# Kernel optimization log

Measured on AMD Instinct MI355X. Metric: run time of the kernel, lower is better.

Reference implementation:

```python
import jax, jax.numpy as jnp
import numpy as np

H = 256      # hidden_dim
NH = 4       # num_heads
DK = H // NH # per-head dim
NL = 2       # num self-attn layers
TL = 6       # transformer_num_layers (output repeat)
PTS_DIM = 3


def _layer_norm(x, g, b, eps=1e-5):
    m = jnp.mean(x, axis=-1, keepdims=True)
    v = jnp.mean((x - m) ** 2, axis=-1, keepdims=True)
    return (x - m) / jnp.sqrt(v + eps) * g + b


def _mha(x, Wq, bq, Wk, bk, Wv, bv, Wo, bo, g, bb, bias):
    # x: [B,N,H]; bias: [B,NH,N,N]; way='add' (att_spm_type='add')
    B, N, _ = x.shape
    q = (x @ Wq + bq).reshape(B, N, NH, DK).transpose(0, 2, 1, 3)  # [B,h,N,d]
    k = (x @ Wk + bk).reshape(B, N, NH, DK).transpose(0, 2, 1, 3)
    v = (x @ Wv + bv).reshape(B, N, NH, DK).transpose(0, 2, 1, 3)
    att = jnp.einsum('bhnd,bhmd->bhnm', q, k) / np.sqrt(DK).astype(np.float32)
    att = jax.nn.softmax(att + bias, axis=-1)
    out = jnp.einsum('bhnm,bhmd->bhnd', att, v).transpose(0, 2, 1, 3).reshape(B, N, H)
    out = out @ Wo + bo
    return _layer_norm(x + out, g, bb)


def setup_inputs() -> dict:
    key = jax.random.key(0)
    ks = jax.random.split(key, 16)
    B, N = 1, 512
    s = 0.02  # weight init scale
    inp = {
        'history_states': jax.random.normal(ks[0], (TL, B, N, H), jnp.float32),
        'all_lanes_preds': jax.random.normal(ks[1], (TL, B, N, 33), jnp.float32),
        'fc_W': jax.random.normal(ks[2], (H, H), jnp.float32) * s,
        'fc_b': jnp.zeros((H,), jnp.float32),
        'Wq': jax.random.normal(ks[3], (NL, H, H), jnp.float32) * s,
        'bq': jnp.zeros((NL, H), jnp.float32),
        'Wk': jax.random.normal(ks[4], (NL, H, H), jnp.float32) * s,
        'bk': jnp.zeros((NL, H), jnp.float32),
        'Wv': jax.random.normal(ks[5], (NL, H, H), jnp.float32) * s,
        'bv': jnp.zeros((NL, H), jnp.float32),
        'Wo': jax.random.normal(ks[6], (NL, H, H), jnp.float32) * s,
        'bo': jnp.zeros((NL, H), jnp.float32),
        'ln_g': jnp.ones((NL, H), jnp.float32),
        'ln_b': jnp.zeros((NL, H), jnp.float32),
        'mlp1_W': jax.random.normal(ks[7], (H, H), jnp.float32) * s,
        'mlp1_b': jnp.zeros((H,), jnp.float32),
        'mlp2_W': jax.random.normal(ks[8], (H, H), jnp.float32) * s,
        'mlp2_b': jnp.zeros((H,), jnp.float32),
        'cls_W1': jax.random.normal(ks[9], (2 * H, H), jnp.float32) * s,
        'cls_b1': jnp.zeros((H,), jnp.float32),
        'cls_W2': jax.random.normal(ks[10], (H, 1), jnp.float32) * s,
        'cls_b2': jnp.zeros((1,), jnp.float32),
    }
    return inp


def reference(history_states, all_lanes_preds, fc_W, fc_b, Wq, bq, Wk, bk, Wv, bv,
              Wo, bo, ln_g, ln_b, mlp1_W, mlp1_b, mlp2_W, mlp2_b,
              cls_W1, cls_b1, cls_W2, cls_b2):
    query_feats = history_states[-1]                 # [B,N,H]
    coords = all_lanes_preds[-1]                      # [B,N,33]
    B, N, C = coords.shape
    coords = coords.reshape(B, N, C // PTS_DIM, PTS_DIM)
    query_end_point = coords[:, :, -1, :]             # [B,N,3]
    key_start_point = coords[:, :, 0, :]              # [B,N,3]

    # pairwise distance bias: dist[b,i,j] = ||key_start[j] - query_end[i]||
    diff = key_start_point[:, None, :, :] - query_end_point[:, :, None, :]
    dist = jnp.sqrt(jnp.sum(diff ** 2, axis=-1))[:, None, :, :]  # [B,1,N,N]
    dw = 1.0 / (dist + 0.01)
    dw = dw / jnp.sum(dw, axis=2, keepdims=True)      # normalize over dim 2
    zeros = jnp.zeros_like(dw)
    dist_weights = jax.lax.stop_gradient(
        jnp.concatenate([dw, -dist, zeros, zeros], axis=1))  # [B,4,N,N]

    # features_concat: Linear + ReLU
    x = jax.nn.relu(query_feats @ fc_W + fc_b)

    for i in range(NL):
        x = _mha(x, Wq[i], bq[i], Wk[i], bk[i], Wv[i], bv[i],
                 Wo[i], bo[i], ln_g[i], ln_b[i], dist_weights)

    # lclc relationship head: per-side MLP, pairwise concat, classifier
    o1 = jax.nn.relu(x @ mlp1_W + mlp1_b)             # [B,N,H]
    o2 = jax.nn.relu(x @ mlp2_W + mlp2_b)
    pair = jnp.concatenate([
        jnp.broadcast_to(o1[:, :, None, :], (B, N, N, H)),
        jnp.broadcast_to(o2[:, None, :, :], (B, N, N, H))], axis=-1)  # [B,N,N,2H]
    z = jax.nn.relu(pair @ cls_W1 + cls_b1)
    lclc = (z @ cls_W2 + cls_b2)[..., 0]              # [B,N,N]
    all_lclc_preds = jnp.broadcast_to(lclc[None], (TL, B, N, N))
    return all_lclc_preds
```

## Files before the change

### kernel.cpp

```cpp
#include <hip/hip_runtime.h>
#include <math.h>


#define NTOK 512
#define HDIM 256
#define DKH  64
#define NHEAD 4
#define TLEN 6
#define WSZ  65536
#define PSTR 520
#define XPS  264

typedef __attribute__((ext_vector_type(8))) short bf16x8;
typedef __attribute__((ext_vector_type(4))) float f32x4;

__device__ __forceinline__ ushort f2bf(float f)
{
    unsigned u = __builtin_bit_cast(unsigned, f);
    u += 0x7FFFu + ((u >> 16) & 1u);
    return (ushort)(u >> 16);
}

struct PKArg {
    const float* w[13];
    const float* pl;
    ushort* wpk;
    float *dist, *dwraw, *inv_cs;
};

__global__ __launch_bounds__(256) void pack_kernel(PKArg p)
{
    __shared__ __align__(16) ushort smu[64 * 72];
    const int bid = blockIdx.x;
    const int t   = threadIdx.x;

    if (bid < 208) {
        const int mat  = bid >> 4;
        const int tile = bid & 15;
        const int k0   = (tile >> 2) * 64;
        const int c0   = (tile & 3) * 64;
        const float* W = p.w[mat];
#pragma unroll
        for (int j = 0; j < 4; ++j) {
            const int i  = t + j * 256;
            const int r  = i >> 4, c4 = i & 15;
            const float4 v4 = *(const float4*)&W[(k0 + r) * HDIM + c0 + c4 * 4];
            smu[(c4 * 4 + 0) * 72 + r] = f2bf(v4.x);
            smu[(c4 * 4 + 1) * 72 + r] = f2bf(v4.y);
            smu[(c4 * 4 + 2) * 72 + r] = f2bf(v4.z);
            smu[(c4 * 4 + 3) * 72 + r] = f2bf(v4.w);
        }
        __syncthreads();
#pragma unroll
        for (int j = 0; j < 2; ++j) {
            const int i  = t + j * 256;
            const int cr = i >> 3, kk = i & 7;
            const uint4 v = *(const uint4*)&smu[cr * 72 + kk * 8];
            *(uint4*)&p.wpk[mat * WSZ + (c0 + cr) * HDIM + k0 + kk * 8] = v;
        }
    } else {
        float* smf = (float*)smu;
        float* qe  = smf;
        float* red = smf + 1536;
        const int item = bid - 208;
        for (int i = t; i < 512; i += 256) {
            qe[i * 3 + 0] = p.pl[i * 33 + 30];
            qe[i * 3 + 1] = p.pl[i * 33 + 31];
            qe[i * 3 + 2] = p.pl[i * 33 + 32];
        }
        __syncthreads();
        const int m   = item * 64 + (t & 63);
        const int nch = t >> 6;
        const float kx = p.pl[m * 33 + 0], ky = p.pl[m * 33 + 1], kz = p.pl[m * 33 + 2];
        float cs = 0.f;
        for (int n = nch * 128; n < nch * 128 + 128; ++n) {
            const float dx = kx - qe[n * 3 + 0];
            const float dy = ky - qe[n * 3 + 1];
            const float dz = kz - qe[n * 3 + 2];
            const float dd = sqrtf(dx * dx + dy * dy + dz * dz);
            const float w  = 1.0f / (dd + 0.01f);
            p.dist[n * NTOK + m]  = dd;
            p.dwraw[n * NTOK + m] = w;
            cs += w;
        }
        red[nch * 64 + (t & 63)] = cs;
        __syncthreads();
        if (t < 64)
            p.inv_cs[item * 64 + t] =
                1.0f / (red[t] + red[64 + t] + red[128 + t] + red[192 + t]);
    }
}

__device__ __forceinline__ void qkv_one2(
    const ushort* __restrict__ xpan, const ushort* __restrict__ Wt,
    const float* __restrict__ bb, int prob,
    int slab, int c0, int lr, int lg, int lk,
    ushort* __restrict__ q16, ushort* __restrict__ k16,
    ushort* __restrict__ vT16)
{
    const ushort* Ap = xpan + lr * XPS + lk;
    f32x4 acc[2];
    acc[0] = (f32x4){0.f, 0.f, 0.f, 0.f};
    acc[1] = (f32x4){0.f, 0.f, 0.f, 0.f};
#pragma unroll
    for (int ks = 0; ks < 8; ++ks) {
        const bf16x8 a = *(const bf16x8*)&Ap[ks * 32];
#pragma unroll
        for (int j = 0; j < 2; ++j) {
            const bf16x8 b = *(const bf16x8*)&Wt[(c0 + j * 16 + lr) * HDIM + ks * 32 + lk];
            acc[j] = __builtin_amdgcn_mfma_f32_16x16x32_bf16(a, b, acc[j], 0, 0, 0);
        }
    }
#pragma unroll
    for (int j = 0; j < 2; ++j) {
        const int col = c0 + j * 16 + lr;
        const float bv2 = bb[col];
        if (prob < 2) {
            ushort* dst = (prob == 0) ? q16 : k16;
#pragma unroll
            for (int rg = 0; rg < 4; ++rg)
                dst[(slab + lg * 4 + rg) * HDIM + col] = f2bf(acc[j][rg] + bv2);
        } else {
            ushort4 s = {f2bf(acc[j][0] + bv2), f2bf(acc[j][1] + bv2),
                         f2bf(acc[j][2] + bv2), f2bf(acc[j][3] + bv2)};
            *(ushort4*)&vT16[col * NTOK + slab + lg * 4] = s;
        }
    }
}

__global__ __launch_bounds__(256) void fcqkv(
    const float* __restrict__ qf, const ushort* __restrict__ fcWt,
    const float* __restrict__ fcb,
    const ushort* __restrict__ WqT, const float* __restrict__ bq,
    const ushort* __restrict__ WkT, const float* __restrict__ bk,
    const ushort* __restrict__ WvT, const float* __restrict__ bv,
    float* __restrict__ xa, ushort* __restrict__ q16,
    ushort* __restrict__ k16, ushort* __restrict__ vT16)
{
    __shared__ __align__(16) ushort xpan[16 * XPS];
    const int bid  = blockIdx.x;
    const int p6   = bid >> 5;
    const int slab = (bid & 31) * 16;
    const int t = threadIdx.x;
    const int wv = t >> 6, lane = t & 63;
    const int lr = lane & 15, lg = lane >> 4, lk = lg * 8;
    const int c0 = wv * 64;

    {
        f32x4 acc[4];
#pragma unroll
        for (int j = 0; j < 4; ++j) acc[j] = (f32x4){0.f, 0.f, 0.f, 0.f};
        const float* Aq = qf + (slab + lr) * HDIM + lk;
#pragma unroll
        for (int ks = 0; ks < 8; ++ks) {
            const float4 a0 = *(const float4*)&Aq[ks * 32];
            const float4 a1 = *(const float4*)&Aq[ks * 32 + 4];
            bf16x8 a;
            a[0] = (short)f2bf(a0.x); a[1] = (short)f2bf(a0.y);
            a[2] = (short)f2bf(a0.z); a[3] = (short)f2bf(a0.w);
            a[4] = (short)f2bf(a1.x); a[5] = (short)f2bf(a1.y);
            a[6] = (short)f2bf(a1.z); a[7] = (short)f2bf(a1.w);
#pragma unroll
            for (int j = 0; j < 4; ++j) {
                const bf16x8 b = *(const bf16x8*)&fcWt[(c0 + j * 16 + lr) * HDIM + ks * 32 + lk];
                acc[j] = __builtin_amdgcn_mfma_f32_16x16x32_bf16(a, b, acc[j], 0, 0, 0);
            }
        }
#pragma unroll
        for (int j = 0; j < 4; ++j) {
            const int col = c0 + j * 16 + lr;
            const float bbv = fcb[col];
#pragma unroll
            for (int rg = 0; rg < 4; ++rg) {
                const float o = fmaxf(acc[j][rg] + bbv, 0.f);
                if (p6 == 0) xa[(slab + lg * 4 + rg) * HDIM + col] = o;
                xpan[(lg * 4 + rg) * XPS + col] = f2bf(o);
            }
        }
    }
    __syncthreads();
    const int prob = p6 >> 1, ch = p6 & 1;
    const ushort* Wt = (prob == 0) ? WqT : (prob == 1) ? WkT : WvT;
    const float*  bb = (prob == 0) ? bq  : (prob == 1) ? bk  : bv;
    qkv_one2(xpan, Wt, bb, prob, slab, ch * 128 + wv * 32, lr, lg, lk,
             q16, k16, vT16);
}

__global__ __launch_bounds__(512) void attn_fused(
    const ushort* __restrict__ q16, const ushort* __restrict__ k16,
    const ushort* __restrict__ vT16, const float* __restrict__ dist,
    const float* __restrict__ dwraw, const float* __restrict__ inv_cs,
    ushort* __restrict__ ao16)
{
    __shared__ __align__(16) ushort P_lds[16 * PSTR];
    __shared__ __align__(16) float exch[8][16][64];
    __shared__ float rmax[8][16];
    __shared__ float psums[8][16];

    const int bid = blockIdx.x;
    const int h  = bid >> 5;
    const int n0 = (bid & 31) * 16;
    const int t  = threadIdx.x;
    const int wv = t >> 6, lane = t & 63;
    const int lr = lane & 15, lg = lane >> 4, lk = lg * 8;
    const int mW = wv * 64;

    const ushort* Qrow = q16 + (n0 + lr) * HDIM + h * DKH + lk;
    const bf16x8 a0 = *(const bf16x8*)&Qrow[0];
    const bf16x8 a1 = *(const bf16x8*)&Qrow[32];

    f32x4 accs[4];
#pragma unroll
    for (int cg = 0; cg < 4; ++cg) accs[cg] = (f32x4){0.f, 0.f, 0.f, 0.f};
#pragma unroll
    for (int cg = 0; cg < 4; ++cg) {
        const ushort* Brow = k16 + (mW + cg * 16 + lr) * HDIM + h * DKH + lk;
        accs[cg] = __builtin_amdgcn_mfma_f32_16x16x32_bf16(
            a0, *(const bf16x8*)&Brow[0], accs[cg], 0, 0, 0);
        accs[cg] = __builtin_amdgcn_mfma_f32_16x16x32_bf16(
            a1, *(const bf16x8*)&Brow[32], accs[cg], 0, 0, 0);
    }

    float s[4][4];
#pragma unroll
    for (int cg = 0; cg < 4; ++cg) {
        const int m = mW + cg * 16 + lr;
        const float ic = (h == 0) ? inv_cs[m] : 0.f;
#pragma unroll
        for (int rg = 0; rg < 4; ++rg) {
            const int n = n0 + lg * 4 + rg;
            float b = 0.f;
            if (h == 0)      b = dwraw[n * NTOK + m] * ic;
            else if (h == 1) b = -dist[n * NTOK + m];
            s[cg][rg] = accs[cg][rg] * 0.125f + b;
        }
    }

    float mx[4];
#pragma unroll
    for (int rg = 0; rg < 4; ++rg) {
        float m = fmaxf(fmaxf(s[0][rg], s[1][rg]), fmaxf(s[2][rg], s[3][rg]));
#pragma unroll
        for (int o = 1; o < 16; o <<= 1) m = fmaxf(m, __shfl_xor(m, o));
        mx[rg] = m;
    }
    if (lr == 0)
#pragma unroll
        for (int rg = 0; rg < 4; ++rg) rmax[wv][lg * 4 + rg] = mx[rg];
    __syncthreads();
    float mxf[4];
#pragma unroll
    for (int rg = 0; rg < 4; ++rg) {
        const int row = lg * 4 + rg;
        float m = rmax[0][row];
#pragma unroll
        for (int w = 1; w < 8; ++w) m = fmaxf(m, rmax[w][row]);
        mxf[rg] = m;
    }

    float ps[4] = {0.f, 0.f, 0.f, 0.f};
#pragma unroll
    for (int cg = 0; cg < 4; ++cg)
#pragma unroll
        for (int rg = 0; rg < 4; ++rg) {
            const float e = __expf(s[cg][rg] - mxf[rg]);
            ps[rg] += e;
            P_lds[(lg * 4 + rg) * PSTR + mW + cg * 16 + lr] = f2bf(e);
        }
#pragma unroll
    for (int rg = 0; rg < 4; ++rg) {
#pragma unroll
        for (int o = 1; o < 16; o <<= 1) ps[rg] += __shfl_xor(ps[rg], o);
    }
    if (lr == 0)
#pragma unroll
        for (int rg = 0; rg < 4; ++rg) psums[wv][lg * 4 + rg] = ps[rg];
    __syncthreads();

    f32x4 acco[4];
#pragma unroll
    for (int db = 0; db < 4; ++db) acco[db] = (f32x4){0.f, 0.f, 0.f, 0.f};
#pragma unroll
    for (int c = 0; c < 2; ++c) {
        const bf16x8 pa = *(const bf16x8*)&P_lds[lr * PSTR + mW + c * 32 + lk];
#pragma unroll
        for (int db = 0; db < 4; ++db) {
            const bf16x8 b = *(const bf16x8*)
                &vT16[(h * DKH + db * 16 + lr) * NTOK + mW + c * 32 + lk];
            acco[db] = __builtin_amdgcn_mfma_f32_16x16x32_bf16(pa, b, acco[db], 0, 0, 0);
        }
    }
#pragma unroll
    for (int db = 0; db < 4; ++db)
#pragma unroll
        for (int rg = 0; rg < 4; ++rg)
            exch[wv][lg * 4 + rg][db * 16 + lr] = acco[db][rg];
    __syncthreads();

    {
        const int r = t >> 5, dp = (t & 31) * 2;
        float sx = 0.f, sy = 0.f, den = 0.f;
#pragma unroll
        for (int w = 0; w < 8; ++w) {
            const float2 e = *(const float2*)&exch[w][r][dp];
            sx += e.x; sy += e.y;
            den += psums[w][r];
        }
        const float inv = 1.0f / den;
        ushort2 o = {f2bf(sx * inv), f2bf(sy * inv)};
        *(ushort2*)&ao16[(n0 + r) * HDIM + h * DKH + dp] = o;
    }
}

__device__ __forceinline__ void oprojln_phase(
    const ushort* __restrict__ ao16, const ushort* __restrict__ WoT,
    const float* __restrict__ bo, const float* __restrict__ gamma,
    const float* __restrict__ beta, const float* __restrict__ x,
    int slab, int c0, int wv, int lr, int lg, int lk,
    float red[4][16], f32x4 acc[4])
{
    const ushort* Arow = ao16 + (slab + lr) * HDIM + lk;
#pragma unroll
    for (int j = 0; j < 4; ++j) acc[j] = (f32x4){0.f, 0.f, 0.f, 0.f};
#pragma unroll
    for (int ks = 0; ks < 8; ++ks) {
        const bf16x8 a = *(const bf16x8*)&Arow[ks * 32];
#pragma unroll
        for (int j = 0; j < 4; ++j) {
            const bf16x8 b = *(const bf16x8*)&WoT[(c0 + j * 16 + lr) * HDIM + ks * 32 + lk];
            acc[j] = __builtin_amdgcn_mfma_f32_16x16x32_bf16(a, b, acc[j], 0, 0, 0);
        }
    }
#pragma unroll
    for (int j = 0; j < 4; ++j) {
        const int col = c0 + j * 16 + lr;
        const float bc = bo[col];
#pragma unroll
        for (int rg = 0; rg < 4; ++rg)
            acc[j][rg] += bc + x[(slab + lg * 4 + rg) * HDIM + col];
    }

    float sm[4];
#pragma unroll
    for (int rg = 0; rg < 4; ++rg) {
        float s = 0.f;
#pragma unroll
        for (int j = 0; j < 4; ++j) s += acc[j][rg];
#pragma unroll
        for (int o = 1; o < 16; o <<= 1) s += __shfl_xor(s, o);
        sm[rg] = s;
    }
    if (lr == 0)
#pragma unroll
        for (int rg = 0; rg < 4; ++rg) red[wv][lg * 4 + rg] = sm[rg];
    __syncthreads();
    float mean[4];
#pragma unroll
    for (int rg = 0; rg < 4; ++rg) {
        const int row = lg * 4 + rg;
        mean[rg] = (red[0][row] + red[1][row] + red[2][row] + red[3][row]) * (1.f / 256.f);
    }
    __syncthreads();

#pragma unroll
    for (int rg = 0; rg < 4; ++rg) {
        float s2 = 0.f;
#pragma unroll
        for (int j = 0; j < 4; ++j) {
            const float c = acc[j][rg] - mean[rg];
            s2 += c * c;
        }
#pragma unroll
        for (int o = 1; o < 16; o <<= 1) s2 += __shfl_xor(s2, o);
        sm[rg] = s2;
    }
    if (lr == 0)
#pragma unroll
        for (int rg = 0; rg < 4; ++rg) red[wv][lg * 4 + rg] = sm[rg];
    __syncthreads();
    float rstd[4];
#pragma unroll
    for (int rg = 0; rg < 4; ++rg) {
        const int row = lg * 4 + rg;
        const float var = (red[0][row] + red[1][row] + red[2][row] + red[3][row]) * (1.f / 256.f);
        rstd[rg] = rsqrtf(var + 1e-5f);
    }
#pragma unroll
    for (int j = 0; j < 4; ++j) {
        const int col = c0 + j * 16 + lr;
        const float gg = gamma[col], bv = beta[col];
#pragma unroll
        for (int rg = 0; rg < 4; ++rg)
            acc[j][rg] = (acc[j][rg] - mean[rg]) * rstd[rg] * gg + bv;
    }
}

__global__ __launch_bounds__(256) void oprojqkv(
    const ushort* __restrict__ ao16, const ushort* __restrict__ WoT,
    const float* __restrict__ bo, const float* __restrict__ gamma,
    const float* __restrict__ beta,
    const ushort* __restrict__ WqT, const float* __restrict__ bq,
    const ushort* __restrict__ WkT, const float* __restrict__ bk,
    const ushort* __restrict__ WvT, const float* __restrict__ bv,
    const float* __restrict__ xa, float* __restrict__ xb,
    ushort* __restrict__ q16, ushort* __restrict__ k16,
    ushort* __restrict__ vT16)
{
    __shared__ __align__(16) ushort xpan[16 * XPS];
    __shared__ float red[4][16];
    const int bid  = blockIdx.x;
    const int p6   = bid >> 5;
    const int slab = (bid & 31) * 16;
    const int t = threadIdx.x;
    const int wv = t >> 6, lane = t & 63;
    const int lr = lane & 15, lg = lane >> 4, lk = lg * 8;
    const int c0 = wv * 64;

    f32x4 acc[4];
    oprojln_phase(ao16, WoT, bo, gamma, beta, xa, slab, c0, wv, lr, lg, lk, red, acc);
#pragma unroll
    for (int j = 0; j < 4; ++j) {
        const int col = c0 + j * 16 + lr;
#pragma unroll
        for (int rg = 0; rg < 4; ++rg) {
            if (p6 == 0) xb[(slab + lg * 4 + rg) * HDIM + col] = acc[j][rg];
            xpan[(lg * 4 + rg) * XPS + col] = f2bf(acc[j][rg]);
        }
    }
    __syncthreads();
    const int prob = p6 >> 1, ch = p6 & 1;
    const ushort* Wt = (prob == 0) ? WqT : (prob == 1) ? WkT : WvT;
    const float*  bb = (prob == 0) ? bq  : (prob == 1) ? bk  : bv;
    qkv_one2(xpan, Wt, bb, prob, slab, ch * 128 + wv * 32, lr, lg, lk,
             q16, k16, vT16);
}

__global__ __launch_bounds__(256) void oprojmlpU(
    const ushort* __restrict__ ao16, const ushort* __restrict__ WoT,
    const float* __restrict__ bo, const float* __restrict__ gamma,
    const float* __restrict__ beta,
    const ushort* __restrict__ m1WT, const float* __restrict__ m1b,
    const ushort* __restrict__ m2WT, const float* __restrict__ m2b,
    const ushort* __restrict__ cW1aT, const float* __restrict__ cb1,
    const ushort* __restrict__ cW1bT,
    const float* __restrict__ xb, float* __restrict__ U1, float* __restrict__ U2)
{
    __shared__ __align__(16) ushort xpan[16 * XPS];
    __shared__ __align__(16) ushort opan[16 * XPS];
    __shared__ float red[4][16];
    const int bid  = blockIdx.x;
    const int p4   = bid >> 5;
    const int p    = p4 >> 1, ch = p4 & 1;
    const int slab = (bid & 31) * 16;
    const int t = threadIdx.x;
    const int wv = t >> 6, lane = t & 63;
    const int lr = lane & 15, lg = lane >> 4, lk = lg * 8;
    const int c0 = wv * 64;

    f32x4 acc[4];
    oprojln_phase(ao16, WoT, bo, gamma, beta, xb, slab, c0, wv, lr, lg, lk, red, acc);
#pragma unroll
    for (int j = 0; j < 4; ++j) {
        const int col = c0 + j * 16 + lr;
#pragma unroll
        for (int rg = 0; rg < 4; ++rg)
            xpan[(lg * 4 + rg) * XPS + col] = f2bf(acc[j][rg]);
    }
    __syncthreads();

    {
        const ushort* Wt = p ? m2WT : m1WT;
        const float*  bb = p ? m2b  : m1b;
        const ushort* Ap = xpan + lr * XPS + lk;
        f32x4 a2[4];
#pragma unroll
        for (int j = 0; j < 4; ++j) a2[j] = (f32x4){0.f, 0.f, 0.f, 0.f};
#pragma unroll
        for (int ks = 0; ks < 8; ++ks) {
            const bf16x8 a = *(const bf16x8*)&Ap[ks * 32];
#pragma unroll
            for (int j = 0; j < 4; ++j) {
                const bf16x8 b = *(const bf16x8*)&Wt[(c0 + j * 16 + lr) * HDIM + ks * 32 + lk];
                a2[j] = __builtin_amdgcn_mfma_f32_16x16x32_bf16(a, b, a2[j], 0, 0, 0);
            }
        }
#pragma unroll
        for (int j = 0; j < 4; ++j) {
            const int col = c0 + j * 16 + lr;
            const float bbv = bb[col];
#pragma unroll
            for (int rg = 0; rg < 4; ++rg)
                opan[(lg * 4 + rg) * XPS + col] = f2bf(fmaxf(a2[j][rg] + bbv, 0.f));
        }
    }
    __syncthreads();

    {
        const ushort* Wt = p ? cW1bT : cW1aT;
        float* U         = p ? U2 : U1;
        const int cb     = ch * 128 + wv * 32;
        const ushort* Ao = opan + lr * XPS + lk;
        f32x4 a2[2];
        a2[0] = (f32x4){0.f, 0.f, 0.f, 0.f};
        a2[1] = (f32x4){0.f, 0.f, 0.f, 0.f};
#pragma unroll
        for (int ks = 0; ks < 8; ++ks) {
            const bf16x8 a = *(const bf16x8*)&Ao[ks * 32];
#pragma unroll
            for (int j = 0; j < 2; ++j) {
                const bf16x8 b = *(const bf16x8*)&Wt[(cb + j * 16 + lr) * HDIM + ks * 32 + lk];
                a2[j] = __builtin_amdgcn_mfma_f32_16x16x32_bf16(a, b, a2[j], 0, 0, 0);
            }
        }
#pragma unroll
        for (int j = 0; j < 2; ++j) {
            const int col = cb + j * 16 + lr;
            const float bbv = (p == 0) ? cb1[col] : 0.f;
#pragma unroll
            for (int rg = 0; rg < 4; ++rg)
                U[(slab + lg * 4 + rg) * HDIM + col] = a2[j][rg] + bbv;
        }
    }
}

__global__ __launch_bounds__(256) void pair_cls(const float* __restrict__ U1,
                                                const float* __restrict__ U2,
                                                const float* __restrict__ W2,
                                                const float* __restrict__ b2,
                                                float* __restrict__ out)
{
    __shared__ __align__(16) float u1s[32][260];
    __shared__ __align__(16) float u2s[32][260];
    __shared__ __align__(16) float w2s[256];
    const int t  = threadIdx.x;
    const int n0 = blockIdx.y * 32, m0 = blockIdx.x * 32;

    for (int i = t; i < 32 * 64; i += 256) {
        const int r = i >> 6, c4 = i & 63;
        *(float4*)&u1s[r][c4 * 4] = *(const float4*)&U1[(n0 + r) * HDIM + c4 * 4];
        *(float4*)&u2s[r][c4 * 4] = *(const float4*)&U2[(m0 + r) * HDIM + c4 * 4];
    }
    if (t < 64) *(float4*)&w2s[t * 4] = *(const float4*)&W2[t * 4];
    __syncthreads();

    const int tx = t & 15, ty = t >> 4;
    float acc[2][2] = {};
    for (int h4 = 0; h4 < 64; ++h4) {
        const float4 a0 = *(const float4*)&u1s[ty * 2][h4 * 4];
        const float4 a1 = *(const float4*)&u1s[ty * 2 + 1][h4 * 4];
        const float4 b0 = *(const float4*)&u2s[tx * 2][h4 * 4];
        const float4 b1 = *(const float4*)&u2s[tx * 2 + 1][h4 * 4];
        const float4 w  = *(const float4*)&w2s[h4 * 4];
#define RT(A, B) fmaxf((A) + (B), 0.f)
        acc[0][0] += RT(a0.x,b0.x)*w.x + RT(a0.y,b0.y)*w.y + RT(a0.z,b0.z)*w.z + RT(a0.w,b0.w)*w.w;
        acc[0][1] += RT(a0.x,b1.x)*w.x + RT(a0.y,b1.y)*w.y + RT(a0.z,b1.z)*w.z + RT(a0.w,b1.w)*w.w;
        acc[1][0] += RT(a1.x,b0.x)*w.x + RT(a1.y,b0.y)*w.y + RT(a1.z,b0.z)*w.z + RT(a1.w,b0.w)*w.w;
        acc[1][1] += RT(a1.x,b1.x)*w.x + RT(a1.y,b1.y)*w.y + RT(a1.z,b1.z)*w.z + RT(a1.w,b1.w)*w.w;
#undef RT
    }
    const float bbv = b2[0];
#pragma unroll
    for (int ii = 0; ii < 2; ++ii)
#pragma unroll
        for (int jj = 0; jj < 2; ++jj) {
            const float val = acc[ii][jj] + bbv;
            const int n = n0 + ty * 2 + ii;
            const int m = m0 + tx * 2 + jj;
#pragma unroll
            for (int tl = 0; tl < TLEN; ++tl)
                out[tl * NTOK * NTOK + n * NTOK + m] = val;
        }
}

extern "C" void kernel_launch(void* const* d_in, const int* in_sizes, int n_in,
                              void* d_out, int out_size, void* d_ws, size_t ws_size,
                              hipStream_t stream)
{
    const float* hs   = (const float*)d_in[0];
    const float* qf   = hs + 5 * NTOK * HDIM;
    const float* alp  = (const float*)d_in[1];
    const float* pl   = alp + 5 * NTOK * 33;
    const float* fc_W = (const float*)d_in[2];
    const float* fc_b = (const float*)d_in[3];
    const float* Wq   = (const float*)d_in[4];
    const float* bq   = (const float*)d_in[5];
    const float* Wk   = (const float*)d_in[6];
    const float* bk   = (const float*)d_in[7];
    const float* Wv   = (const float*)d_in[8];
    const float* bv   = (const float*)d_in[9];
    const float* Wo   = (const float*)d_in[10];
    const float* bo   = (const float*)d_in[11];
    const float* lng  = (const float*)d_in[12];
    const float* lnb  = (const float*)d_in[13];
    const float* m1W  = (const float*)d_in[14];
    const float* m1b  = (const float*)d_in[15];
    const float* m2W  = (const float*)d_in[16];
    const float* m2b  = (const float*)d_in[17];
    const float* cW1  = (const float*)d_in[18];
    const float* cb1  = (const float*)d_in[19];
    const float* cW2  = (const float*)d_in[20];
    const float* cb2  = (const float*)d_in[21];
    float* out = (float*)d_out;

    const int NN  = NTOK * NTOK;
    const int NH_ = NTOK * HDIM;
    float* ws     = (float*)d_ws;
    float* dist   = ws;
    float* dwraw  = ws + NN;
    float* inv_cs = ws + 2 * NN;
    float* xa     = ws + 2 * NN + 512;
    float* xb     = xa + NH_;
    float* U1     = xb + NH_;
    float* U2     = U1 + NH_;
    ushort* u16   = (ushort*)(U2 + NH_);
    ushort* wpk   = u16;
    ushort* q16   = wpk + 13 * WSZ;
    ushort* k16   = q16 + NH_;
    ushort* vT16  = k16 + NH_;
    ushort* ao16  = vT16 + NH_;

    PKArg pk;
    pk.w[0]  = fc_W;
    pk.w[1]  = Wq;  pk.w[2]  = Wq + WSZ;
    pk.w[3]  = Wk;  pk.w[4]  = Wk + WSZ;
    pk.w[5]  = Wv;  pk.w[6]  = Wv + WSZ;
    pk.w[7]  = Wo;  pk.w[8]  = Wo + WSZ;
    pk.w[9]  = m1W; pk.w[10] = m2W;
    pk.w[11] = cW1; pk.w[12] = cW1 + WSZ;
    pk.pl = pl;
    pk.wpk = wpk;
    pk.dist = dist; pk.dwraw = dwraw; pk.inv_cs = inv_cs;
    pack_kernel<<<216, 256, 0, stream>>>(pk);

    fcqkv<<<192, 256, 0, stream>>>(
        qf, wpk + 0 * WSZ, fc_b,
        wpk + 1 * WSZ, bq, wpk + 3 * WSZ, bk, wpk + 5 * WSZ, bv,
        xa, q16, k16, vT16);

    attn_fused<<<128, 512, 0, stream>>>(q16, k16, vT16, dist, dwraw, inv_cs, ao16);

    oprojqkv<<<192, 256, 0, stream>>>(
        ao16, wpk + 7 * WSZ, bo, lng, lnb,
        wpk + 2 * WSZ, bq + HDIM, wpk + 4 * WSZ, bk + HDIM,
        wpk + 6 * WSZ, bv + HDIM,
        xa, xb, q16, k16, vT16);

    attn_fused<<<128, 512, 0, stream>>>(q16, k16, vT16, dist, dwraw, inv_cs, ao16);

    oprojmlpU<<<128, 256, 0, stream>>>(
        ao16, wpk + 8 * WSZ, bo + HDIM, lng + HDIM, lnb + HDIM,
        wpk + 9 * WSZ, m1b, wpk + 10 * WSZ, m2b,
        wpk + 11 * WSZ, cb1, wpk + 12 * WSZ,
        xb, U1, U2);

    pair_cls<<<dim3(16, 16), 256, 0, stream>>>(U1, U2, cW2, cb2, out);
}
```

Before: 97.69 us.

## Store pair-head U1/U2 as bf16 and repartition attention PV across waves

The U1/U2 intermediates produced by oprojmlpU are now stored as bf16 and unpacked to fp32 in pair_cls. This halves their global traffic and the LDS footprint of the pair tile, at some cost in precision. In attn_fused, each wave now owns one 16-column slice of the head dim over half of the keys instead of all 64 columns over 64 keys. That shrinks the cross-wave exchange buffer from 8 partials to 2 and uses wider final stores. The change trades more unpack ALU work in the pair loop for less memory and LDS traffic.

```diff
diff --git a/kernel.cpp b/kernel.cpp
--- a/kernel.cpp
+++ b/kernel.cpp
@@ -19,6 +19,14 @@
     unsigned u = __builtin_bit_cast(unsigned, f);
     u += 0x7FFFu + ((u >> 16) & 1u);
     return (ushort)(u >> 16);
+}
+__device__ __forceinline__ float bf_lo(unsigned u)
+{
+    return __builtin_bit_cast(float, u << 16);
+}
+__device__ __forceinline__ float bf_hi(unsigned u)
+{
+    return __builtin_bit_cast(float, u & 0xFFFF0000u);
 }
 
 struct PKArg {
@@ -193,7 +201,7 @@
     ushort* __restrict__ ao16)
 {
     __shared__ __align__(16) ushort P_lds[16 * PSTR];
-    __shared__ __align__(16) float exch[8][16][64];
+    __shared__ __align__(16) float exch[2][16][64];
     __shared__ float rmax[8][16];
     __shared__ float psums[8][16];
 
@@ -277,38 +285,34 @@
         for (int rg = 0; rg < 4; ++rg) psums[wv][lg * 4 + rg] = ps[rg];
     __syncthreads();
 
-    f32x4 acco[4];
-#pragma unroll
-    for (int db = 0; db < 4; ++db) acco[db] = (f32x4){0.f, 0.f, 0.f, 0.f};
-#pragma unroll
-    for (int c = 0; c < 2; ++c) {
-        const bf16x8 pa = *(const bf16x8*)&P_lds[lr * PSTR + mW + c * 32 + lk];
-#pragma unroll
-        for (int db = 0; db < 4; ++db) {
-            const bf16x8 b = *(const bf16x8*)
-                &vT16[(h * DKH + db * 16 + lr) * NTOK + mW + c * 32 + lk];
-            acco[db] = __builtin_amdgcn_mfma_f32_16x16x32_bf16(pa, b, acco[db], 0, 0, 0);
-        }
-    }
-#pragma unroll
-    for (int db = 0; db < 4; ++db)
+    {
+        const int db = wv & 3, kh = wv >> 2;
+        f32x4 acco = (f32x4){0.f, 0.f, 0.f, 0.f};
+        const ushort* Vrow = vT16 + (h * DKH + db * 16 + lr) * NTOK + kh * 256 + lk;
+        const ushort* Prow = P_lds + lr * PSTR + kh * 256 + lk;
+#pragma unroll
+        for (int c = 0; c < 8; ++c) {
+            const bf16x8 pa = *(const bf16x8*)&Prow[c * 32];
+            const bf16x8 b  = *(const bf16x8*)&Vrow[c * 32];
+            acco = __builtin_amdgcn_mfma_f32_16x16x32_bf16(pa, b, acco, 0, 0, 0);
+        }
 #pragma unroll
         for (int rg = 0; rg < 4; ++rg)
-            exch[wv][lg * 4 + rg][db * 16 + lr] = acco[db][rg];
-    __syncthreads();
-
-    {
-        const int r = t >> 5, dp = (t & 31) * 2;
-        float sx = 0.f, sy = 0.f, den = 0.f;
-#pragma unroll
-        for (int w = 0; w < 8; ++w) {
-            const float2 e = *(const float2*)&exch[w][r][dp];
-            sx += e.x; sy += e.y;
-            den += psums[w][r];
-        }
+            exch[kh][lg * 4 + rg][db * 16 + lr] = acco[rg];
+    }
+    __syncthreads();
+
+    if (t < 256) {
+        const int r = t >> 4, d4 = t & 15;
+        f32x4 sum = *(const f32x4*)&exch[0][r][d4 * 4];
+        sum += *(const f32x4*)&exch[1][r][d4 * 4];
+        float den = 0.f;
+#pragma unroll
+        for (int w = 0; w < 8; ++w) den += psums[w][r];
         const float inv = 1.0f / den;
-        ushort2 o = {f2bf(sx * inv), f2bf(sy * inv)};
-        *(ushort2*)&ao16[(n0 + r) * HDIM + h * DKH + dp] = o;
+        ushort4 o = {f2bf(sum.x * inv), f2bf(sum.y * inv),
+                     f2bf(sum.z * inv), f2bf(sum.w * inv)};
+        *(ushort4*)&ao16[(n0 + r) * HDIM + h * DKH + d4 * 4] = o;
     }
 }
 
@@ -443,7 +447,8 @@
     const ushort* __restrict__ m2WT, const float* __restrict__ m2b,
     const ushort* __restrict__ cW1aT, const float* __restrict__ cb1,
     const ushort* __restrict__ cW1bT,
-    const float* __restrict__ xb, float* __restrict__ U1, float* __restrict__ U2)
+    const float* __restrict__ xb, ushort* __restrict__ U1b,
+    ushort* __restrict__ U2b)
 {
     __shared__ __align__(16) ushort xpan[16 * XPS];
     __shared__ __align__(16) ushort opan[16 * XPS];
@@ -497,7 +502,7 @@
 
     {
         const ushort* Wt = p ? cW1bT : cW1aT;
-        float* U         = p ? U2 : U1;
+        ushort* U        = p ? U2b : U1b;
         const int cb     = ch * 128 + wv * 32;
         const ushort* Ao = opan + lr * XPS + lk;
         f32x4 a2[2];
@@ -518,46 +523,68 @@
             const float bbv = (p == 0) ? cb1[col] : 0.f;
 #pragma unroll
             for (int rg = 0; rg < 4; ++rg)
-                U[(slab + lg * 4 + rg) * HDIM + col] = a2[j][rg] + bbv;
-        }
-    }
-}
-
-__global__ __launch_bounds__(256) void pair_cls(const float* __restrict__ U1,
-                                                const float* __restrict__ U2,
+                U[(slab + lg * 4 + rg) * HDIM + col] = f2bf(a2[j][rg] + bbv);
+        }
+    }
+}
+
+__global__ __launch_bounds__(256) void pair_cls(const ushort* __restrict__ U1b,
+                                                const ushort* __restrict__ U2b,
                                                 const float* __restrict__ W2,
                                                 const float* __restrict__ b2,
                                                 float* __restrict__ out)
 {
-    __shared__ __align__(16) float u1s[32][260];
-    __shared__ __align__(16) float u2s[32][260];
+    __shared__ __align__(16) ushort u1s[32][264];
+    __shared__ __align__(16) ushort u2s[32][264];
     __shared__ __align__(16) float w2s[256];
     const int t  = threadIdx.x;
     const int n0 = blockIdx.y * 32, m0 = blockIdx.x * 32;
 
-    for (int i = t; i < 32 * 64; i += 256) {
-        const int r = i >> 6, c4 = i & 63;
-        *(float4*)&u1s[r][c4 * 4] = *(const float4*)&U1[(n0 + r) * HDIM + c4 * 4];
-        *(float4*)&u2s[r][c4 * 4] = *(const float4*)&U2[(m0 + r) * HDIM + c4 * 4];
+#pragma unroll
+    for (int u = 0; u < 4; ++u) {
+        const int i = t + u * 256;
+        const int r = i >> 5, c8 = i & 31;
+        *(uint4*)&u1s[r][c8 * 8] = *(const uint4*)&U1b[(n0 + r) * HDIM + c8 * 8];
+        *(uint4*)&u2s[r][c8 * 8] = *(const uint4*)&U2b[(m0 + r) * HDIM + c8 * 8];
     }
     if (t < 64) *(float4*)&w2s[t * 4] = *(const float4*)&W2[t * 4];
     __syncthreads();
 
     const int tx = t & 15, ty = t >> 4;
+    const ushort* r0 = &u1s[ty * 2][0];
+    const ushort* r1 = &u1s[ty * 2 + 1][0];
+    const ushort* c0 = &u2s[tx * 2][0];
+    const ushort* c1 = &u2s[tx * 2 + 1][0];
     float acc[2][2] = {};
-    for (int h4 = 0; h4 < 64; ++h4) {
-        const float4 a0 = *(const float4*)&u1s[ty * 2][h4 * 4];
-        const float4 a1 = *(const float4*)&u1s[ty * 2 + 1][h4 * 4];
-        const float4 b0 = *(const float4*)&u2s[tx * 2][h4 * 4];
-        const float4 b1 = *(const float4*)&u2s[tx * 2 + 1][h4 * 4];
-        const float4 w  = *(const float4*)&w2s[h4 * 4];
+
 #define RT(A, B) fmaxf((A) + (B), 0.f)
-        acc[0][0] += RT(a0.x,b0.x)*w.x + RT(a0.y,b0.y)*w.y + RT(a0.z,b0.z)*w.z + RT(a0.w,b0.w)*w.w;
-        acc[0][1] += RT(a0.x,b1.x)*w.x + RT(a0.y,b1.y)*w.y + RT(a0.z,b1.z)*w.z + RT(a0.w,b1.w)*w.w;
-        acc[1][0] += RT(a1.x,b0.x)*w.x + RT(a1.y,b0.y)*w.y + RT(a1.z,b0.z)*w.z + RT(a1.w,b0.w)*w.w;
-        acc[1][1] += RT(a1.x,b1.x)*w.x + RT(a1.y,b1.y)*w.y + RT(a1.z,b1.z)*w.z + RT(a1.w,b1.w)*w.w;
+    for (int h8 = 0; h8 < 32; ++h8) {
+        const uint4 A0 = *(const uint4*)&r0[h8 * 8];
+        const uint4 A1 = *(const uint4*)&r1[h8 * 8];
+        const uint4 B0 = *(const uint4*)&c0[h8 * 8];
+        const uint4 B1 = *(const uint4*)&c1[h8 * 8];
+        const float4 w0 = *(const float4*)&w2s[h8 * 8];
+        const float4 w1 = *(const float4*)&w2s[h8 * 8 + 4];
+        const float warr[8] = {w0.x, w0.y, w0.z, w0.w, w1.x, w1.y, w1.z, w1.w};
+#pragma unroll
+        for (int q = 0; q < 4; ++q) {
+            const unsigned a0u = ((const unsigned*)&A0)[q];
+            const unsigned a1u = ((const unsigned*)&A1)[q];
+            const unsigned b0u = ((const unsigned*)&B0)[q];
+            const unsigned b1u = ((const unsigned*)&B1)[q];
+            const float a0l = bf_lo(a0u), a0h = bf_hi(a0u);
+            const float a1l = bf_lo(a1u), a1h = bf_hi(a1u);
+            const float b0l = bf_lo(b0u), b0h = bf_hi(b0u);
+            const float b1l = bf_lo(b1u), b1h = bf_hi(b1u);
+            const float wl = warr[q * 2], wh = warr[q * 2 + 1];
+            acc[0][0] += RT(a0l, b0l) * wl + RT(a0h, b0h) * wh;
+            acc[0][1] += RT(a0l, b1l) * wl + RT(a0h, b1h) * wh;
+            acc[1][0] += RT(a1l, b0l) * wl + RT(a1h, b0h) * wh;
+            acc[1][1] += RT(a1l, b1l) * wl + RT(a1h, b1h) * wh;
+        }
+    }
 #undef RT
-    }
+
     const float bbv = b2[0];
 #pragma unroll
     for (int ii = 0; ii < 2; ++ii)
@@ -610,14 +637,14 @@
     float* inv_cs = ws + 2 * NN;
     float* xa     = ws + 2 * NN + 512;
     float* xb     = xa + NH_;
-    float* U1     = xb + NH_;
-    float* U2     = U1 + NH_;
-    ushort* u16   = (ushort*)(U2 + NH_);
+    ushort* u16   = (ushort*)(xb + NH_);
     ushort* wpk   = u16;
     ushort* q16   = wpk + 13 * WSZ;
     ushort* k16   = q16 + NH_;
     ushort* vT16  = k16 + NH_;
     ushort* ao16  = vT16 + NH_;
+    ushort* U1b   = ao16 + NH_;
+    ushort* U2b   = U1b + NH_;
 
     PKArg pk;
     pk.w[0]  = fc_W;
@@ -651,7 +678,7 @@
         ao16, wpk + 8 * WSZ, bo + HDIM, lng + HDIM, lnb + HDIM,
         wpk + 9 * WSZ, m1b, wpk + 10 * WSZ, m2b,
         wpk + 11 * WSZ, cb1, wpk + 12 * WSZ,
-        xb, U1, U2);
-
-    pair_cls<<<dim3(16, 16), 256, 0, stream>>>(U1, U2, cW2, cb2, out);
-}
+        xb, U1b, U2b);
+
+    pair_cls<<<dim3(16, 16), 256, 0, stream>>>(U1b, U2b, cW2, cb2, out);
+}
```

After: 95.66 us. -2.1%, faster.
